# Kernel optimization log

Hardware: AMD Instinct MI355X
Metric: run time of the kernel (lower is better)

Reference implementation:

```python
import jax, jax.numpy as jnp
import numpy as np
from jax import lax

EPS = 1e-6

def _ln(x):
    # LayerNorm32 over channel dim, computed in fp32
    x32 = x.astype(jnp.float32)
    mu = jnp.mean(x32, axis=-1, keepdims=True)
    var = jnp.mean(jnp.square(x32 - mu), axis=-1, keepdims=True)
    return ((x32 - mu) * lax.rsqrt(var + EPS)).astype(x.dtype)

def _downsample2(f, mask):
    # mean over active voxels in each 2x2x2 cell; f must already be zero at inactive voxels
    B, D, H, W, C = f.shape
    fs = f.reshape(B, D // 2, 2, H // 2, 2, W // 2, 2, C).sum(axis=(2, 4, 6))
    cnt = mask.reshape(B, D // 2, 2, H // 2, 2, W // 2, 2).astype(f.dtype).sum(axis=(2, 4, 6))
    out = fs / jnp.maximum(cnt, 1.0)[..., None]
    return out, cnt > 0

def _subm_conv3(x, w, b, mask_f):
    # submanifold sparse conv == dense SAME conv on zero-filled grid, masked to active set
    y = lax.conv_general_dilated(x, w, window_strides=(1, 1, 1), padding='SAME',
                                 dimension_numbers=('NDHWC', 'DHWIO', 'NDHWC'))
    return (y + b) * mask_f


def setup_inputs() -> dict:
    key = jax.random.key(0)
    ks = jax.random.split(key, 6)
    B, D, C, CO = 4, 64, 64, 128
    feats = jax.random.normal(ks[0], (B, D, D, D, C), jnp.float32)
    mask = jax.random.uniform(ks[1], (B, D, D, D)) < 0.3
    gamma1 = jnp.ones((C,), jnp.float32)
    beta1 = jnp.zeros((C,), jnp.float32)
    w1 = jax.random.normal(ks[2], (3, 3, 3, C, CO), jnp.float32) / np.sqrt(27.0 * C)
    b1 = jnp.zeros((CO,), jnp.float32)
    # conv2 is zero-initialized in the original (zero_module); we use small random
    # weights so the reference is numerically non-degenerate
    w2 = jax.random.normal(ks[3], (3, 3, 3, CO, CO), jnp.float32) / np.sqrt(27.0 * CO)
    b2 = jnp.zeros((CO,), jnp.float32)
    w_skip = jax.random.normal(ks[4], (C, CO), jnp.float32) / np.sqrt(C)
    b_skip = jnp.zeros((CO,), jnp.float32)
    return dict(feats=feats, mask=mask, gamma1=gamma1, beta1=beta1,
                w1=w1, b1=b1, w2=w2, b2=b2, w_skip=w_skip, b_skip=b_skip)


def reference(feats, mask, gamma1, beta1, w1, b1, w2, b2, w_skip, b_skip):
    m = mask[..., None].astype(feats.dtype)          # [B,D,H,W,1]
    h = (_ln(feats) * gamma1 + beta1)                # norm1 (affine)
    h = jax.nn.silu(h) * m                           # silu, restrict to active set
    xm = feats * m
    h, mask2 = _downsample2(h, mask)                 # SparseDownsample(2) on h
    x_ds, _ = _downsample2(xm, mask)                 # SparseDownsample(2) on x
    m2 = mask2[..., None].astype(feats.dtype)
    h = _subm_conv3(h, w1, b1, m2)                   # conv1
    h = jax.nn.silu(_ln(h)) * m2                     # norm2 (no affine) + silu
    h = _subm_conv3(h, w2, b2, m2)                   # conv2
    skip = (x_ds @ w_skip + b_skip) * m2             # SparseLinear skip
    return h + skip
```

## Files before the change

### kernel.cpp

```cpp
#include <hip/hip_runtime.h>
#include <hip/hip_bf16.h>

#define EPS 1e-6f
typedef unsigned short b16;
typedef __attribute__((ext_vector_type(8))) short v8s;
typedef __attribute__((ext_vector_type(4))) float v4f;

typedef const __attribute__((address_space(1))) void* gptr_t;
typedef __attribute__((address_space(3))) void* lptr_t;

__device__ __forceinline__ b16 f2b(float f) {
    __hip_bfloat16 h = __float2bfloat16(f);
    return *reinterpret_cast<b16*>(&h);
}
__device__ __forceinline__ float siluf(float x){ return x / (1.f + __expf(-x)); }

__device__ __forceinline__ void gll16(const b16* g, b16* l) {
    __builtin_amdgcn_global_load_lds((gptr_t)g, (lptr_t)l, 16, 0, 0);
}

__device__ __forceinline__ float red64(float s) {
    int t;
    t = __builtin_amdgcn_update_dpp(0, __float_as_int(s), 0x121, 0xF, 0xF, false);
    s += __int_as_float(t);
    t = __builtin_amdgcn_update_dpp(0, __float_as_int(s), 0x122, 0xF, 0xF, false);
    s += __int_as_float(t);
    t = __builtin_amdgcn_update_dpp(0, __float_as_int(s), 0x124, 0xF, 0xF, false);
    s += __int_as_float(t);
    t = __builtin_amdgcn_update_dpp(0, __float_as_int(s), 0x128, 0xF, 0xF, false);
    s += __int_as_float(t);
    s += __int_as_float(__builtin_amdgcn_ds_swizzle(__float_as_int(s), 0x401F));
    s += __shfl_xor(s, 32, 64);
    return s;
}

template<int IC>
__global__ void __launch_bounds__(256) k_wt(const float* __restrict__ w, b16* __restrict__ o, int tot) {
    int i = blockIdx.x*256 + threadIdx.x;
    if (i >= tot) return;
    int ic = i % IC; int oc = (i / IC) & 127; int tap = i / (IC*128);
    o[i] = f2b(w[(tap*IC + ic)*128 + oc]);
}

template<int IC>
__global__ void __launch_bounds__(256) k_wtb(const float* __restrict__ w, b16* __restrict__ o, int tot) {
    int i = blockIdx.x*256 + threadIdx.x;
    if (i >= tot) return;
    constexpr int ICB = IC/32;
    int icl = i & 31;
    int oc  = (i >> 5) & 127;
    int r   = i >> 12;
    int tap = r / ICB, icb = r % ICB;
    o[i] = f2b(w[(tap*IC + icb*32 + icl)*128 + oc]);
}

__global__ void __launch_bounds__(256) k_ln_down(
    const float* __restrict__ feats, const int* __restrict__ mask,
    const float* __restrict__ gamma, const float* __restrict__ beta,
    b16* __restrict__ h_ds_pad, b16* __restrict__ x_ds, float* __restrict__ cnt_out)
{
    int wave = (blockIdx.x * 256 + threadIdx.x) >> 6;
    int lane = threadIdx.x & 63;
    int x = wave & 31, y = (wave >> 5) & 31, z = (wave >> 10) & 31, b = wave >> 15;
    float g = gamma[lane], be = beta[lane];
    float hacc = 0.f, xacc = 0.f, cnt = 0.f;
    #pragma unroll
    for (int i = 0; i < 8; ++i) {
        int zz = 2*z + (i>>2), yy = 2*y + ((i>>1)&1), xx = 2*x + (i&1);
        int vox = ((b*64 + zz)*64 + yy)*64 + xx;
        int m = mask[vox];
        float val = feats[vox*64 + lane];
        float s1 = red64(val);
        float s2 = red64(val*val);
        float mu = s1 * (1.f/64.f);
        float var = fmaxf(s2 * (1.f/64.f) - mu*mu, 0.f);
        float h = (val - mu) * rsqrtf(var + EPS) * g + be;
        h = siluf(h);
        if (m != 0) { hacc += h; xacc += val; cnt += 1.f; }
    }
    float inv = 1.f / fmaxf(cnt, 1.f);
    long vp = ((long)(b*34 + z+1)*34 + (y+1))*34 + (x+1);
    h_ds_pad[vp*64 + lane] = f2b(hacc * inv);
    x_ds[(long)wave*64 + lane] = f2b(xacc * inv);
    if (lane == 0) cnt_out[wave] = cnt;
}

template<int IC, bool IS_CONV1>
__device__ __forceinline__ void conv_body(
    const b16* __restrict__ inp,
    const b16* __restrict__ wt,
    const float* __restrict__ bias,
    const float* __restrict__ cnt,
    const b16* __restrict__ x_ds,
    const b16* __restrict__ wst,
    const float* __restrict__ b_skip,
    b16* __restrict__ h2out,
    float* __restrict__ out)
{
    constexpr int ICB = IC/32;
    constexpr int NK = 27*ICB;
    __shared__ b16 lA[2][4096];
    __shared__ b16 lB[2][4096];

    int bid = ((blockIdx.x & 7) << 7) | (blockIdx.x >> 3);
    int y0 = (bid & 7) << 2;
    int z  = (bid >> 3) & 31;
    int b  = bid >> 8;
    int t  = threadIdx.x;
    int lane = t & 63;
    int w = t >> 6;
    int col = lane & 15;
    int quad = lane >> 4;

    const b16* gAsrc[2];
    const b16* gBsrc[2];
    {
        int vsub = lane >> 2;
        int s    = lane & 3;
        #pragma unroll
        for (int j = 0; j < 2; ++j) {
            int x  = j*16 + vsub;
            int cA = (s - (x >> 1)) & 3;
            gAsrc[j] = inp + ((long)((b*34 + z)*34 + (y0 + w))*34 + x)*IC + cA*8;
            int oc = w*32 + j*16 + vsub;
            int cB = (s - (vsub >> 1)) & 3;
            gBsrc[j] = wt + oc*32 + cB*8;
        }
    }

    int so   = ((quad + (col>>1)) & 3) * 8;
    int aoff = w*1024 + col*32 + so;
    int boff = col*32 + so;

    v4f acc[2][8];
    #pragma unroll
    for (int tl=0;tl<2;++tl)
        #pragma unroll
        for (int n=0;n<8;++n) acc[tl][n] = (v4f){0.f,0.f,0.f,0.f};

    long offAn = 0;
    int icbn = 0, kxn = 0, kyn = 0;
    auto advance = [&]() {
        ++icbn; offAn += 32;
        if (icbn == ICB) {
            icbn = 0;
            ++kxn;
            if (kxn == 3) {
                kxn = 0; ++kyn;
                if (kyn == 3) { kyn = 0; offAn += (long)(34*34 - 2*34 - 3)*IC; }
                else          {           offAn += (long)(34 - 3)*IC; }
            }
        }
    };

    auto stage = [&](long offA, long offB, int buf) {
        #pragma unroll
        for (int j = 0; j < 2; ++j) {
            gll16(gAsrc[j] + offA, &lA[buf][w*1024 + j*512]);
            gll16(gBsrc[j] + offB, &lB[buf][w*1024 + j*512]);
        }
    };

    stage(0, 0, 0);
    advance();
    long offBn = 4096;
    __syncthreads();

    int cur = 0;
    for (int k = 0; k < NK; ++k) {
        if (k + 1 < NK) {
            stage(offAn, offBn, cur ^ 1);
            advance();
            offBn += 4096;
        }
        v8s a0 = *(const v8s*)(&lA[cur][aoff]);
        v8s a1 = *(const v8s*)(&lA[cur][aoff + 512]);
        #pragma unroll
        for (int n = 0; n < 8; ++n) {
            v8s bb = *(const v8s*)(&lB[cur][n*512 + boff]);
            acc[0][n] = __builtin_amdgcn_mfma_f32_16x16x32_bf16(a0, bb, acc[0][n], 0,0,0);
            acc[1][n] = __builtin_amdgcn_mfma_f32_16x16x32_bf16(a1, bb, acc[1][n], 0,0,0);
        }
        __syncthreads();
        cur ^= 1;
    }

    int yrow = y0 + w;
    long cellrow = ((long)(b*32+z)*32 + yrow)*32;

    if (!IS_CONV1) {
        const b16* X0 = x_ds + (cellrow + col)*64 + quad*8;
        const b16* X1 = X0 + 16*64;
        const b16* WS = wst + col*64 + quad*8;
        #pragma unroll
        for (int s = 0; s < 2; ++s) {
            v8s a0 = *(const v8s*)(X0 + s*32);
            v8s a1 = *(const v8s*)(X1 + s*32);
            #pragma unroll
            for (int n=0;n<8;++n) {
                v8s bb = *(const v8s*)(WS + n*16*64 + s*32);
                acc[0][n] = __builtin_amdgcn_mfma_f32_16x16x32_bf16(a0, bb, acc[0][n], 0,0,0);
                acc[1][n] = __builtin_amdgcn_mfma_f32_16x16x32_bf16(a1, bb, acc[1][n], 0,0,0);
            }
        }
    }

    float bv[8];
    #pragma unroll
    for (int n=0;n<8;++n)
        bv[n] = bias[n*16+col] + (IS_CONV1 ? 0.f : b_skip[n*16+col]);

    long prow = ((long)(b*34 + z+1)*34 + (yrow+1))*34 + 1;

    #pragma unroll
    for (int tl=0; tl<2; ++tl) {
        if (IS_CONV1) {
            float s1[4], s2[4];
            #pragma unroll
            for (int r=0;r<4;++r){
                float a=0.f, q=0.f;
                #pragma unroll
                for (int n=0;n<8;++n){ float v = acc[tl][n][r] + bv[n]; a+=v; q+=v*v; }
                s1[r]=a; s2[r]=q;
            }
            #pragma unroll
            for (int off=1; off<16; off<<=1){
                #pragma unroll
                for (int r=0;r<4;++r){ s1[r]+=__shfl_xor(s1[r],off); s2[r]+=__shfl_xor(s2[r],off); }
            }
            #pragma unroll
            for (int r=0;r<4;++r){
                int row = quad*4 + r;
                int x = tl*16 + row;
                float c = cnt[cellrow + x];
                float mu = s1[r]*(1.f/128.f);
                float var = fmaxf(s2[r]*(1.f/128.f) - mu*mu, 0.f);
                float rs = rsqrtf(var + EPS);
                bool act = c > 0.f;
                #pragma unroll
                for (int n=0;n<8;++n){
                    float v = acc[tl][n][r] + bv[n];
                    float hv = act ? siluf((v-mu)*rs) : 0.f;
                    h2out[(prow + x)*128 + n*16 + col] = f2b(hv);
                }
            }
        } else {
            #pragma unroll
            for (int r=0;r<4;++r){
                int row = quad*4 + r;
                int x = tl*16 + row;
                float c = cnt[cellrow + x];
                bool act = c > 0.f;
                #pragma unroll
                for (int n=0;n<8;++n){
                    float v = acc[tl][n][r] + bv[n];
                    out[(cellrow + x)*128 + n*16 + col] = act ? v : 0.f;
                }
            }
        }
    }
}

__global__ void __launch_bounds__(256, 4) k_conv1(
    const b16* __restrict__ inp, const b16* __restrict__ wt,
    const float* __restrict__ bias, const float* __restrict__ cnt,
    b16* __restrict__ h2out)
{
    conv_body<64, true>(inp, wt, bias, cnt, nullptr, nullptr, nullptr, h2out, nullptr);
}

__global__ void __launch_bounds__(256, 4) k_conv2(
    const b16* __restrict__ inp, const b16* __restrict__ wt,
    const float* __restrict__ bias, const float* __restrict__ cnt,
    const b16* __restrict__ x_ds, const b16* __restrict__ wst,
    const float* __restrict__ b_skip, float* __restrict__ out)
{
    conv_body<128, false>(inp, wt, bias, cnt, x_ds, wst, b_skip, nullptr, out);
}

extern "C" void kernel_launch(void* const* d_in, const int* in_sizes, int n_in,
                              void* d_out, int out_size, void* d_ws, size_t ws_size,
                              hipStream_t stream) {
    const float* feats  = (const float*)d_in[0];
    const int*   mask   = (const int*)  d_in[1];
    const float* gamma1 = (const float*)d_in[2];
    const float* beta1  = (const float*)d_in[3];
    const float* w1     = (const float*)d_in[4];
    const float* b1     = (const float*)d_in[5];
    const float* w2     = (const float*)d_in[6];
    const float* b2     = (const float*)d_in[7];
    const float* w_skip = (const float*)d_in[8];
    const float* b_skip = (const float*)d_in[9];
    float* out = (float*)d_out;

    char* ws = (char*)d_ws;
    b16*   h_ds_pad = (b16*)(ws);
    b16*   h2_pad   = (b16*)(ws + 20123648);
    b16*   x_ds     = (b16*)(ws + 60370944);
    float* cnt      = (float*)(ws + 77148160);
    b16*   w1t      = (b16*)(ws + 77672448);
    b16*   w2t      = (b16*)(ws + 78114816);
    b16*   wst      = (b16*)(ws + 78999552);

    hipMemsetAsync(h_ds_pad, 0, 20123648, stream);
    hipMemsetAsync(h2_pad,   0, 40247296, stream);

    const int n_w1 = 27*64*128;
    const int n_w2 = 27*128*128;
    const int n_ws = 64*128;
    k_wtb<64> <<<(n_w1 + 255)/256, 256, 0, stream>>>(w1, w1t, n_w1);
    k_wtb<128><<<(n_w2 + 255)/256, 256, 0, stream>>>(w2, w2t, n_w2);
    k_wt<64>  <<<(n_ws + 255)/256, 256, 0, stream>>>(w_skip, wst, n_ws);

    k_ln_down<<<32768, 256, 0, stream>>>(feats, mask, gamma1, beta1, h_ds_pad, x_ds, cnt);

    k_conv1<<<1024, 256, 0, stream>>>(h_ds_pad, w1t, b1, cnt, h2_pad);
    k_conv2<<<1024, 256, 0, stream>>>(h2_pad, w2t, b2, cnt, x_ds, wst, b_skip, out);
}
```

Before: 621.8 us.

## Use 2x2 wave tiling in conv2 and skip LN work on inactive voxels

The templated conv body is split into separate conv1 and conv2 kernels. conv2 now gives each wave a 64x64 output tile (4 row tiles by 4 column tiles) instead of 32x128, so each k-step does 8 LDS fragment loads rather than 10 for the same 16 MFMAs, and the skip GEMM and epilogue are remapped to match. Separately, the LN/downsample kernel now loads features and runs the reductions only for active voxels, which saves memory traffic and DPP work on the roughly 70% of voxels that are inactive. The change adds branch divergence at wave level, but the mask value is uniform across a wave, so the branch is uniform.

```diff
diff --git a/kernel.cpp b/kernel.cpp
--- a/kernel.cpp
+++ b/kernel.cpp
@@ -69,14 +69,16 @@
         int zz = 2*z + (i>>2), yy = 2*y + ((i>>1)&1), xx = 2*x + (i&1);
         int vox = ((b*64 + zz)*64 + yy)*64 + xx;
         int m = mask[vox];
-        float val = feats[vox*64 + lane];
-        float s1 = red64(val);
-        float s2 = red64(val*val);
-        float mu = s1 * (1.f/64.f);
-        float var = fmaxf(s2 * (1.f/64.f) - mu*mu, 0.f);
-        float h = (val - mu) * rsqrtf(var + EPS) * g + be;
-        h = siluf(h);
-        if (m != 0) { hacc += h; xacc += val; cnt += 1.f; }
+        if (m != 0) {
+            float val = feats[vox*64 + lane];
+            float s1 = red64(val);
+            float s2 = red64(val*val);
+            float mu = s1 * (1.f/64.f);
+            float var = fmaxf(s2 * (1.f/64.f) - mu*mu, 0.f);
+            float h = (val - mu) * rsqrtf(var + EPS) * g + be;
+            h = siluf(h);
+            hacc += h; xacc += val; cnt += 1.f;
+        }
     }
     float inv = 1.f / fmaxf(cnt, 1.f);
     long vp = ((long)(b*34 + z+1)*34 + (y+1))*34 + (x+1);
@@ -85,20 +87,14 @@
     if (lane == 0) cnt_out[wave] = cnt;
 }
 
-template<int IC, bool IS_CONV1>
-__device__ __forceinline__ void conv_body(
+__global__ void __launch_bounds__(256, 4) k_conv1(
     const b16* __restrict__ inp,
     const b16* __restrict__ wt,
     const float* __restrict__ bias,
     const float* __restrict__ cnt,
-    const b16* __restrict__ x_ds,
-    const b16* __restrict__ wst,
-    const float* __restrict__ b_skip,
-    b16* __restrict__ h2out,
-    float* __restrict__ out)
+    b16* __restrict__ h2out)
 {
-    constexpr int ICB = IC/32;
-    constexpr int NK = 27*ICB;
+    constexpr int IC = 64, ICB = 2, NK = 54;
     __shared__ b16 lA[2][4096];
     __shared__ b16 lB[2][4096];
 
@@ -122,9 +118,8 @@
             int x  = j*16 + vsub;
             int cA = (s - (x >> 1)) & 3;
             gAsrc[j] = inp + ((long)((b*34 + z)*34 + (y0 + w))*34 + x)*IC + cA*8;
-            int oc = w*32 + j*16 + vsub;
             int cB = (s - (vsub >> 1)) & 3;
-            gBsrc[j] = wt + oc*32 + cB*8;
+            gBsrc[j] = wt + (w*32 + j*16 + vsub)*32 + cB*8;
         }
     }
 
@@ -143,8 +138,7 @@
     auto advance = [&]() {
         ++icbn; offAn += 32;
         if (icbn == ICB) {
-            icbn = 0;
-            ++kxn;
+            icbn = 0; ++kxn;
             if (kxn == 3) {
                 kxn = 0; ++kyn;
                 if (kyn == 3) { kyn = 0; offAn += (long)(34*34 - 2*34 - 3)*IC; }
@@ -152,7 +146,6 @@
             }
         }
     };
-
     auto stage = [&](long offA, long offB, int buf) {
         #pragma unroll
         for (int j = 0; j < 2; ++j) {
@@ -168,11 +161,7 @@
 
     int cur = 0;
     for (int k = 0; k < NK; ++k) {
-        if (k + 1 < NK) {
-            stage(offAn, offBn, cur ^ 1);
-            advance();
-            offBn += 4096;
-        }
+        if (k + 1 < NK) { stage(offAn, offBn, cur ^ 1); advance(); offBn += 4096; }
         v8s a0 = *(const v8s*)(&lA[cur][aoff]);
         v8s a1 = *(const v8s*)(&lA[cur][aoff + 512]);
         #pragma unroll
@@ -188,94 +177,181 @@
     int yrow = y0 + w;
     long cellrow = ((long)(b*32+z)*32 + yrow)*32;
 
-    if (!IS_CONV1) {
-        const b16* X0 = x_ds + (cellrow + col)*64 + quad*8;
-        const b16* X1 = X0 + 16*64;
-        const b16* WS = wst + col*64 + quad*8;
-        #pragma unroll
-        for (int s = 0; s < 2; ++s) {
-            v8s a0 = *(const v8s*)(X0 + s*32);
-            v8s a1 = *(const v8s*)(X1 + s*32);
-            #pragma unroll
-            for (int n=0;n<8;++n) {
-                v8s bb = *(const v8s*)(WS + n*16*64 + s*32);
-                acc[0][n] = __builtin_amdgcn_mfma_f32_16x16x32_bf16(a0, bb, acc[0][n], 0,0,0);
-                acc[1][n] = __builtin_amdgcn_mfma_f32_16x16x32_bf16(a1, bb, acc[1][n], 0,0,0);
-            }
-        }
-    }
-
     float bv[8];
     #pragma unroll
-    for (int n=0;n<8;++n)
-        bv[n] = bias[n*16+col] + (IS_CONV1 ? 0.f : b_skip[n*16+col]);
+    for (int n=0;n<8;++n) bv[n] = bias[n*16+col];
 
     long prow = ((long)(b*34 + z+1)*34 + (yrow+1))*34 + 1;
 
     #pragma unroll
     for (int tl=0; tl<2; ++tl) {
-        if (IS_CONV1) {
-            float s1[4], s2[4];
-            #pragma unroll
-            for (int r=0;r<4;++r){
-                float a=0.f, q=0.f;
+        float s1[4], s2[4];
+        #pragma unroll
+        for (int r=0;r<4;++r){
+            float a=0.f, q=0.f;
+            #pragma unroll
+            for (int n=0;n<8;++n){ float v = acc[tl][n][r] + bv[n]; a+=v; q+=v*v; }
+            s1[r]=a; s2[r]=q;
+        }
+        #pragma unroll
+        for (int off=1; off<16; off<<=1){
+            #pragma unroll
+            for (int r=0;r<4;++r){ s1[r]+=__shfl_xor(s1[r],off); s2[r]+=__shfl_xor(s2[r],off); }
+        }
+        #pragma unroll
+        for (int r=0;r<4;++r){
+            int row = quad*4 + r;
+            int x = tl*16 + row;
+            float c = cnt[cellrow + x];
+            float mu = s1[r]*(1.f/128.f);
+            float var = fmaxf(s2[r]*(1.f/128.f) - mu*mu, 0.f);
+            float rs = rsqrtf(var + EPS);
+            bool act = c > 0.f;
+            #pragma unroll
+            for (int n=0;n<8;++n){
+                float v = acc[tl][n][r] + bv[n];
+                float hv = act ? siluf((v-mu)*rs) : 0.f;
+                h2out[(prow + x)*128 + n*16 + col] = f2b(hv);
+            }
+        }
+    }
+}
+
+__global__ void __launch_bounds__(256, 4) k_conv2(
+    const b16* __restrict__ inp,
+    const b16* __restrict__ wt,
+    const float* __restrict__ bias,
+    const float* __restrict__ cnt,
+    const b16* __restrict__ x_ds,
+    const b16* __restrict__ wst,
+    const float* __restrict__ b_skip,
+    float* __restrict__ out)
+{
+    constexpr int IC = 128, ICB = 4, NK = 108;
+    __shared__ b16 lA[2][4096];
+    __shared__ b16 lB[2][4096];
+
+    int bid = ((blockIdx.x & 7) << 7) | (blockIdx.x >> 3);
+    int y0 = (bid & 7) << 2;
+    int z  = (bid >> 3) & 31;
+    int b  = bid >> 8;
+    int t  = threadIdx.x;
+    int lane = t & 63;
+    int w = t >> 6;
+    int col = lane & 15;
+    int quad = lane >> 4;
+    int wr = w >> 1;
+    int wc = w & 1;
+
+    const b16* gAsrc[2];
+    const b16* gBsrc[2];
+    {
+        int vsub = lane >> 2;
+        int s    = lane & 3;
+        #pragma unroll
+        for (int j = 0; j < 2; ++j) {
+            int x  = j*16 + vsub;
+            int cA = (s - (x >> 1)) & 3;
+            gAsrc[j] = inp + ((long)((b*34 + z)*34 + (y0 + w))*34 + x)*IC + cA*8;
+            int cB = (s - (vsub >> 1)) & 3;
+            gBsrc[j] = wt + (w*32 + j*16 + vsub)*32 + cB*8;
+        }
+    }
+
+    int so   = ((quad + (col>>1)) & 3) * 8;
+    int aoff = wr*2048 + col*32 + so;
+    int boff = wc*2048 + col*32 + so;
+
+    v4f acc[4][4];
+    #pragma unroll
+    for (int rt=0;rt<4;++rt)
+        #pragma unroll
+        for (int ct=0;ct<4;++ct) acc[rt][ct] = (v4f){0.f,0.f,0.f,0.f};
+
+    long offAn = 0;
+    int icbn = 0, kxn = 0, kyn = 0;
+    auto advance = [&]() {
+        ++icbn; offAn += 32;
+        if (icbn == ICB) {
+            icbn = 0; ++kxn;
+            if (kxn == 3) {
+                kxn = 0; ++kyn;
+                if (kyn == 3) { kyn = 0; offAn += (long)(34*34 - 2*34 - 3)*IC; }
+                else          {           offAn += (long)(34 - 3)*IC; }
+            }
+        }
+    };
+    auto stage = [&](long offA, long offB, int buf) {
+        #pragma unroll
+        for (int j = 0; j < 2; ++j) {
+            gll16(gAsrc[j] + offA, &lA[buf][w*1024 + j*512]);
+            gll16(gBsrc[j] + offB, &lB[buf][w*1024 + j*512]);
+        }
+    };
+
+    stage(0, 0, 0);
+    advance();
+    long offBn = 4096;
+    __syncthreads();
+
+    int cur = 0;
+    for (int k = 0; k < NK; ++k) {
+        if (k + 1 < NK) { stage(offAn, offBn, cur ^ 1); advance(); offBn += 4096; }
+        v8s a[4], bb[4];
+        #pragma unroll
+        for (int rt = 0; rt < 4; ++rt) a[rt]  = *(const v8s*)(&lA[cur][aoff + rt*512]);
+        #pragma unroll
+        for (int ct = 0; ct < 4; ++ct) bb[ct] = *(const v8s*)(&lB[cur][boff + ct*512]);
+        #pragma unroll
+        for (int ct = 0; ct < 4; ++ct)
+            #pragma unroll
+            for (int rt = 0; rt < 4; ++rt)
+                acc[rt][ct] = __builtin_amdgcn_mfma_f32_16x16x32_bf16(a[rt], bb[ct], acc[rt][ct], 0,0,0);
+        __syncthreads();
+        cur ^= 1;
+    }
+
+    long cell0 = ((long)(b*32 + z)*32 + y0)*32;
+
+    {
+        const b16* WS = wst + (wc*64 + col)*64 + quad*8;
+        #pragma unroll
+        for (int rt = 0; rt < 4; ++rt) {
+            const b16* X = x_ds + (cell0 + wr*64 + rt*16 + col)*64 + quad*8;
+            #pragma unroll
+            for (int s = 0; s < 2; ++s) {
+                v8s a = *(const v8s*)(X + s*32);
                 #pragma unroll
-                for (int n=0;n<8;++n){ float v = acc[tl][n][r] + bv[n]; a+=v; q+=v*v; }
-                s1[r]=a; s2[r]=q;
-            }
-            #pragma unroll
-            for (int off=1; off<16; off<<=1){
-                #pragma unroll
-                for (int r=0;r<4;++r){ s1[r]+=__shfl_xor(s1[r],off); s2[r]+=__shfl_xor(s2[r],off); }
-            }
-            #pragma unroll
-            for (int r=0;r<4;++r){
-                int row = quad*4 + r;
-                int x = tl*16 + row;
-                float c = cnt[cellrow + x];
-                float mu = s1[r]*(1.f/128.f);
-                float var = fmaxf(s2[r]*(1.f/128.f) - mu*mu, 0.f);
-                float rs = rsqrtf(var + EPS);
-                bool act = c > 0.f;
-                #pragma unroll
-                for (int n=0;n<8;++n){
-                    float v = acc[tl][n][r] + bv[n];
-                    float hv = act ? siluf((v-mu)*rs) : 0.f;
-                    h2out[(prow + x)*128 + n*16 + col] = f2b(hv);
+                for (int ct = 0; ct < 4; ++ct) {
+                    v8s bb = *(const v8s*)(WS + ct*16*64 + s*32);
+                    acc[rt][ct] = __builtin_amdgcn_mfma_f32_16x16x32_bf16(a, bb, acc[rt][ct], 0,0,0);
                 }
             }
-        } else {
-            #pragma unroll
-            for (int r=0;r<4;++r){
-                int row = quad*4 + r;
-                int x = tl*16 + row;
-                float c = cnt[cellrow + x];
-                bool act = c > 0.f;
-                #pragma unroll
-                for (int n=0;n<8;++n){
-                    float v = acc[tl][n][r] + bv[n];
-                    out[(cellrow + x)*128 + n*16 + col] = act ? v : 0.f;
-                }
-            }
-        }
-    }
-}
-
-__global__ void __launch_bounds__(256, 4) k_conv1(
-    const b16* __restrict__ inp, const b16* __restrict__ wt,
-    const float* __restrict__ bias, const float* __restrict__ cnt,
-    b16* __restrict__ h2out)
-{
-    conv_body<64, true>(inp, wt, bias, cnt, nullptr, nullptr, nullptr, h2out, nullptr);
-}
-
-__global__ void __launch_bounds__(256, 4) k_conv2(
-    const b16* __restrict__ inp, const b16* __restrict__ wt,
-    const float* __restrict__ bias, const float* __restrict__ cnt,
-    const b16* __restrict__ x_ds, const b16* __restrict__ wst,
-    const float* __restrict__ b_skip, float* __restrict__ out)
-{
-    conv_body<128, false>(inp, wt, bias, cnt, x_ds, wst, b_skip, nullptr, out);
+        }
+    }
+
+    float bv[4];
+    #pragma unroll
+    for (int ct = 0; ct < 4; ++ct) {
+        int oc = wc*64 + ct*16 + col;
+        bv[ct] = bias[oc] + b_skip[oc];
+    }
+
+    #pragma unroll
+    for (int rt = 0; rt < 4; ++rt) {
+        #pragma unroll
+        for (int r = 0; r < 4; ++r) {
+            int v = wr*64 + rt*16 + quad*4 + r;
+            long cell = cell0 + v;
+            float c = cnt[cell];
+            bool act = c > 0.f;
+            #pragma unroll
+            for (int ct = 0; ct < 4; ++ct) {
+                float vv = acc[rt][ct][r] + bv[ct];
+                out[cell*128 + wc*64 + ct*16 + col] = act ? vv : 0.f;
+            }
+        }
+    }
 }
 
 extern "C" void kernel_launch(void* const* d_in, const int* in_sizes, int n_in,
```

Measured after the change: 632.8 us. No clear change (+1.8%).
